# Kernel optimization log

Hardware: AMD Instinct MI355X
Metric: run time of the kernel (lower is better)

Reference implementation:

```python
import jax, jax.numpy as jnp
import numpy as np
import math

B, H, S, D = 2, 16, 2048, 72
D12 = D // 12  # freq dim per head per component
L_PREFIX, L_SEQ = 576, 512
THETA_T = 100.0


def _make_freqs():
    n = H * D12
    log_min, log_max = math.log(math.pi), math.log(10.0 * math.pi)
    f = jnp.exp(jnp.linspace(log_min, log_max, n + 1)[:-1])  # (H*D12,)
    freqs = jnp.stack([f, f]).reshape(2, D12, H)
    freqs = jnp.swapaxes(freqs, -1, -2)  # (2, H, D12)
    t = THETA_T ** (-jnp.arange(n, dtype=jnp.float32) / n)
    t_freqs = t.reshape(D12, H).T  # (H, D12)
    return freqs.astype(jnp.float32), t_freqs.astype(jnp.float32)


def setup_inputs() -> dict:
    key = jax.random.key(0)
    ks = jax.random.split(key, 8)
    freqs, t_freqs = _make_freqs()
    return {
        "q": jax.random.normal(ks[0], (B, H, S, D), dtype=jnp.float32),
        "k": jax.random.normal(ks[1], (B, H, S, D), dtype=jnp.float32),
        "v": jax.random.normal(ks[2], (B, H, S, D), dtype=jnp.float32),
        "pos": jax.random.uniform(ks[3], (B, S, 2), dtype=jnp.float32),
        "pos_orig": jax.random.uniform(ks[4], (B, S, 2), dtype=jnp.float32),
        "time": jax.random.uniform(ks[5], (B, S), dtype=jnp.float32),
        "freqs": freqs,
        "t_freqs": t_freqs,
        "scale": jax.random.uniform(ks[6], (H, 1, 1), dtype=jnpp_f32()) if False else jax.random.uniform(ks[6], (H, 1, 1), dtype=jnp.float32) + 0.5,
        "l_prefix": L_PREFIX,
        "l_seq": L_SEQ,
    }


def jnp_f32():
    return jnp.float32


def _fp_rope_theta(pos, pos_orig, time, freqs, t_freqs):
    # FPRoPE.forward: theta per token, per head. (B,S,H,5*D12)
    p = jnp.stack([pos_orig, pos], axis=2) * 2.0 - 1.0  # (B,S,2,2)
    th_w = p[..., 0][:, :, :, None, None] * freqs[0]  # (B,S,2,H,D12)
    th_h = p[..., 1][:, :, :, None, None] * freqs[1]  # (B,S,2,H,D12)
    th_t = time[:, :, None, None, None] * t_freqs      # (B,S,1,H,D12)
    theta = jnp.concatenate([th_h, th_w, th_t], axis=2)  # (B,S,5,H,D12)
    theta = jnp.transpose(theta, (0, 3, 1, 2, 4)).reshape(B, H, S, 5 * D12)
    return theta


def _apply_rotary(x, theta):
    d = theta.shape[-1]
    x1, x2, x3 = x[..., :d], x[..., d:2 * d], x[..., 2 * d:]
    c, s = jnp.cos(theta), jnp.sin(theta)
    return jnp.concatenate([x1 * c - x2 * s, x2 * c + x1 * s, x3], axis=-1)


def _block_mask(l_prefix, l_seq):
    # inference_query_causal_mask_mod: prefix attends to nothing; pokes causal;
    # queries attend to prefix+pokes (and self via qn==kn).
    idx = jnp.arange(S)
    qn = (idx - l_prefix)[:, None]
    kn = (idx - l_prefix)[None, :]
    return (qn >= 0) & ((qn == kn) | ((qn >= kn) & (qn < l_seq)) | ((kn < l_seq) & (qn >= l_seq)))


def reference(q, k, v, pos, pos_orig, time, freqs, t_freqs, scale, l_prefix, l_seq):
    theta = _fp_rope_theta(pos, pos_orig, time, freqs, t_freqs)
    q = _apply_rotary(q, theta)
    k = _apply_rotary(k, theta)
    # cosine-similarity QK rescaling (scale_for_cosine_sim)
    eps = 1e-6
    ss = jnp.sqrt(scale)  # (H,1,1) broadcasts over (B,H,S,1)
    q = q * (ss * jax.lax.rsqrt(jnp.sum(q * q, axis=-1, keepdims=True) + eps))
    k = k * (ss * jax.lax.rsqrt(jnp.sum(k * k, axis=-1, keepdims=True) + eps))
    mask = _block_mask(l_prefix, l_seq)  # (S,S)
    scores = jnp.einsum('bhqd,bhkd->bhqk', q, k)
    scores = jnp.where(mask, scores, jnp.float32(-1e30))
    probs = jax.nn.softmax(scores, axis=-1)
    # fully-masked rows (prefix queries) output zeros, matching flex_attention
    row_valid = jnp.any(mask, axis=-1)  # (S,)
    probs = jnp.where(row_valid[None, None, :, None], probs, 0.0)
    return jnp.einsum('bhqk,bhkd->bhqd', probs, v)
```

## Files before the change

kernel.cpp:

```cpp
#include <hip/hip_runtime.h>
#include <math.h>

#define B_ 2
#define H_ 16
#define S_ 2048
#define D_ 72
#define LP 576
#define WEND 1088
#define DP 96
#define DV 80
#define NQ (S_ - LP)

#define CBW 2688
#define LDSW (CBW + 128 + 32)

#define NPREP2 (B_ * H_ * S_ / 8)
#define NVT    (32 * B_ * H_)

typedef __bf16 bf16x8 __attribute__((ext_vector_type(8)));
typedef float f32x4 __attribute__((ext_vector_type(4)));

static __device__ __forceinline__ unsigned pack2bf(float a, float b) {
    __bf16 x = (__bf16)a, y = (__bf16)b;
    unsigned short ux = __builtin_bit_cast(unsigned short, x);
    unsigned short uy = __builtin_bit_cast(unsigned short, y);
    return (unsigned)ux | ((unsigned)uy << 16);
}

static __device__ __forceinline__ f32x4 mfma16(bf16x8 a, bf16x8 b, f32x4 c) {
    return __builtin_amdgcn_mfma_f32_16x16x32_bf16(a, b, c, 0, 0, 0);
}

__global__ __launch_bounds__(256) void pre_kernel(
    const float* __restrict__ q, const float* __restrict__ k,
    const float* __restrict__ v,
    const float* __restrict__ pos, const float* __restrict__ pos_orig,
    const float* __restrict__ time_, const float* __restrict__ freqs,
    const float* __restrict__ t_freqs, const float* __restrict__ scale,
    unsigned* __restrict__ qn, unsigned* __restrict__ kn,
    unsigned short* __restrict__ vt, float* __restrict__ out)
{
    __shared__ __align__(16) float tile[64 * 77];
    if (blockIdx.x < NPREP2) {
        unsigned short* shp = (unsigned short*)tile;
        const int wave = threadIdx.x >> 6;
        const int lane = threadIdx.x & 63;
        const int j = lane & 31;
        const int rw = wave * 2 + (lane >> 5);
        const int row = blockIdx.x * 8 + rw;
        const int s = row & (S_ - 1);
        const int h = (row >> 11) & (H_ - 1);
        const int b = row >> 15;
        const long base = (long)row * D_;
        const int p2 = (b * S_ + s) * 2;

        float oq1 = 0.f, oq2 = 0.f, ok1 = 0.f, ok2 = 0.f;
        float pq[6], pk[6];
        float ssq = 0.f, ssk = 0.f;
        if (j < 30) {
            const float x1q = q[base + j], x2q = q[base + j + 30];
            const float x1k = k[base + j], x2k = k[base + j + 30];
            const int g = j / 6, i = j - 6 * g;
            const float fh = freqs[96 + h * 6 + i];
            const float fw = freqs[h * 6 + i];
            const float ft = t_freqs[h * 6 + i];
            const float f  = (g < 2) ? fh : ((g < 4) ? fw : ft);
            const float by_o = pos_orig[p2 + 1] * 2.f - 1.f;
            const float by_p = pos[p2 + 1]      * 2.f - 1.f;
            const float bx_o = pos_orig[p2 + 0] * 2.f - 1.f;
            const float bx_p = pos[p2 + 0]      * 2.f - 1.f;
            const float bt   = time_[b * S_ + s];
            const float bv = (g == 0) ? by_o : (g == 1) ? by_p :
                             (g == 2) ? bx_o : (g == 3) ? bx_p : bt;
            float sn, cs;
            __sincosf(bv * f, &sn, &cs);
            oq1 = x1q * cs - x2q * sn;  oq2 = x2q * cs + x1q * sn;
            ok1 = x1k * cs - x2k * sn;  ok2 = x2k * cs + x1k * sn;
            ssq = oq1 * oq1 + oq2 * oq2;
            ssk = ok1 * ok1 + ok2 * ok2;
        } else {
            const int e0 = 60 + 6 * (j - 30);
            #pragma unroll
            for (int m = 0; m < 3; ++m) {
                const float2 a = *(const float2*)(q + base + e0 + 2 * m);
                const float2 c = *(const float2*)(k + base + e0 + 2 * m);
                pq[2 * m] = a.x; pq[2 * m + 1] = a.y;
                pk[2 * m] = c.x; pk[2 * m + 1] = c.y;
                ssq += a.x * a.x + a.y * a.y;
                ssk += c.x * c.x + c.y * c.y;
            }
        }
        #pragma unroll
        for (int m = 1; m < 32; m <<= 1) { ssq += __shfl_xor(ssq, m); ssk += __shfl_xor(ssk, m); }
        const float ss = sqrtf(scale[h]);
        const float fq = ss * rsqrtf(ssq + 1e-6f);
        const float fk = ss * rsqrtf(ssk + 1e-6f);

        unsigned short* sq_ = shp + rw * 96;
        unsigned short* sk_ = shp + 768 + rw * 96;
        if (j < 30) {
            sq_[j]      = __builtin_bit_cast(unsigned short, (__bf16)(oq1 * fq));
            sq_[j + 30] = __builtin_bit_cast(unsigned short, (__bf16)(oq2 * fq));
            sk_[j]      = __builtin_bit_cast(unsigned short, (__bf16)(ok1 * fk));
            sk_[j + 30] = __builtin_bit_cast(unsigned short, (__bf16)(ok2 * fk));
        } else {
            const int e0 = 60 + 6 * (j - 30);
            #pragma unroll
            for (int m = 0; m < 6; ++m) {
                sq_[e0 + m] = __builtin_bit_cast(unsigned short, (__bf16)(pq[m] * fq));
                sk_[e0 + m] = __builtin_bit_cast(unsigned short, (__bf16)(pk[m] * fk));
            }
        }
        __syncthreads();
        const int t = threadIdx.x;
        if (t < 192) {
            const int arr = t / 96, rem = t - arr * 96;
            const int rr = rem / 12, seg = rem - rr * 12;
            uint4 val = make_uint4(0u, 0u, 0u, 0u);
            if (seg < 9) val = ((const uint4*)(shp + arr * 768 + rr * 96))[seg];
            unsigned* dst = (arr ? kn : qn) + ((long)(blockIdx.x * 8 + rr)) * 48;
            ((uint4*)dst)[seg] = val;
        }
    } else {
        const int bx2 = blockIdx.x - NPREP2;
        const int st = bx2 & 31, bh = bx2 >> 5;
        const int s0 = st * 64;
        const int t = threadIdx.x;
        if (st < 9) {
            float4* o4 = (float4*)(out + (long)(bh * S_ + s0) * D_);
            for (int i = t; i < 1152; i += 256) o4[i] = make_float4(0.f, 0.f, 0.f, 0.f);
        }
        for (int i = t; i < 1152; i += 256) {
            const int r = i / 18, c = i - r * 18;
            const float4 g = ((const float4*)v)[((long)(bh * S_ + s0 + r) * 18) + c];
            float* d = &tile[r * 77 + c * 4];
            d[0] = g.x; d[1] = g.y; d[2] = g.z; d[3] = g.w;
        }
        __syncthreads();
        for (int i = t; i < 1280; i += 256) {
            const int dd = i >> 4, s4 = i & 15;
            float f0 = 0.f, f1 = 0.f, f2 = 0.f, f3 = 0.f;
            if (dd < D_) {
                f0 = tile[(s4 * 4 + 0) * 77 + dd];
                f1 = tile[(s4 * 4 + 1) * 77 + dd];
                f2 = tile[(s4 * 4 + 2) * 77 + dd];
                f3 = tile[(s4 * 4 + 3) * 77 + dd];
            }
            uint2 o; o.x = pack2bf(f0, f1); o.y = pack2bf(f2, f3);
            ((uint2*)vt)[((((long)bh * DV + dd) << 11) + s0 + s4 * 4) >> 2] = o;
        }
    }
}

__global__ __launch_bounds__(256) void attn_kernel(
    const unsigned short* __restrict__ qn, const unsigned short* __restrict__ kn,
    const unsigned short* __restrict__ vt, float* __restrict__ out)
{
    __shared__ __align__(16) unsigned lds[LDSW];
    const int bh = blockIdx.y;
    const int q0 = LP + blockIdx.x * 32;
    const int tid = threadIdx.x;
    const int w = tid >> 6, lane = tid & 63;
    const int quad = lane >> 4, l16 = lane & 15;
    const bool causal = (q0 < WEND);
    const int ntiles = causal ? ((q0 + 159) >> 7) : 9;

    const unsigned short* qn_b = qn + (((long)bh) << 11) * DP;
    const unsigned short* kn_b = kn + (((long)bh) << 11) * DP;
    const unsigned short* vt_b = vt + (long)bh * DV * S_;

    bf16x8 qf[2][3];
    #pragma unroll
    for (int m = 0; m < 2; ++m)
        #pragma unroll
        for (int c = 0; c < 3; ++c)
            qf[m][c] = *(const bf16x8*)(qn_b + (long)(q0 + 16 * m + l16) * DP + c * 32 + quad * 8);

    f32x4 o[2][5];
    float den[2][4];
    #pragma unroll
    for (int m = 0; m < 2; ++m) {
        #pragma unroll
        for (int dt = 0; dt < 5; ++dt) { o[m][dt][0]=0.f; o[m][dt][1]=0.f; o[m][dt][2]=0.f; o[m][dt][3]=0.f; }
        #pragma unroll
        for (int r = 0; r < 4; ++r) den[m][r] = 0.f;
    }

    unsigned short* Pw = (unsigned short*)lds + w * 640;

    for (int kt = 0; kt < ntiles; ++kt) {
        const int kb = kt * 128 + 32 * w;
        const bool masked = (kt == ntiles - 1);
        bf16x8 kf[2][3], vf[5];
        #pragma unroll
        for (int g = 0; g < 2; ++g)
            #pragma unroll
            for (int c = 0; c < 3; ++c)
                kf[g][c] = *(const bf16x8*)(kn_b + (long)(kb + 16 * g + l16) * DP + c * 32 + quad * 8);
        #pragma unroll
        for (int dt = 0; dt < 5; ++dt)
            vf[dt] = *(const bf16x8*)(vt_b + (((long)(dt * 16 + l16)) << 11) + kb + quad * 8);

        #pragma unroll
        for (int m = 0; m < 2; ++m) {
            f32x4 acc0, acc1;
            acc0[0]=0.f; acc0[1]=0.f; acc0[2]=0.f; acc0[3]=0.f;
            acc1[0]=0.f; acc1[1]=0.f; acc1[2]=0.f; acc1[3]=0.f;
            __builtin_amdgcn_s_setprio(1);
            #pragma unroll
            for (int c = 0; c < 3; ++c) {
                acc0 = mfma16(qf[m][c], kf[0][c], acc0);
                acc1 = mfma16(qf[m][c], kf[1][c], acc1);
            }
            __builtin_amdgcn_s_setprio(0);
            #pragma unroll
            for (int g = 0; g < 2; ++g) {
                const int ka = kb + 16 * g + l16;
                #pragma unroll
                for (int r = 0; r < 4; ++r) {
                    const int qa = q0 + 16 * m + quad * 4 + r;
                    float p = g ? acc1[r] : acc0[r];
                    float e = __expf(p);
                    if (masked) {
                        const bool valid = causal ? (ka <= qa) : (ka < WEND);
                        if (!valid) e = 0.f;
                    }
                    const __bf16 pb = (__bf16)e;
                    den[m][r] += (float)pb;
                    Pw[(quad * 4 + r) * 40 + 16 * g + l16] = __builtin_bit_cast(unsigned short, pb);
                }
            }
            const bf16x8 pa = *(const bf16x8*)(Pw + l16 * 40 + quad * 8);
            __builtin_amdgcn_s_setprio(1);
            #pragma unroll
            for (int dt = 0; dt < 5; ++dt)
                o[m][dt] = mfma16(pa, vf[dt], o[m][dt]);
            __builtin_amdgcn_s_setprio(0);
        }
    }

    #pragma unroll
    for (int m = 0; m < 2; ++m)
        #pragma unroll
        for (int r = 0; r < 4; ++r)
            #pragma unroll
            for (int x = 1; x < 16; x <<= 1) den[m][r] += __shfl_xor(den[m][r], x);

    __syncthreads();
    float* cb  = (float*)lds;
    float* db  = (float*)lds + CBW;
    float* PsD = (float*)lds + CBW + 128;
    if (l16 == 0)
        #pragma unroll
        for (int m = 0; m < 2; ++m)
            #pragma unroll
            for (int r = 0; r < 4; ++r)
                db[w * 32 + 16 * m + quad * 4 + r] = den[m][r];

    float ofin[5][2];
    #pragma unroll
    for (int dt = 0; dt < 5; ++dt) {
        __syncthreads();
        #pragma unroll
        for (int m = 0; m < 2; ++m)
            #pragma unroll
            for (int r = 0; r < 4; ++r)
                cb[w * 672 + (16 * m + quad * 4 + r) * 21 + l16] = o[m][dt][r];
        __syncthreads();
        #pragma unroll
        for (int r = 0; r < 2; ++r) {
            const int row = 8 * w + quad * 2 + r;
            ofin[dt][r] = cb[row * 21 + l16] + cb[672 + row * 21 + l16]
                        + cb[1344 + row * 21 + l16] + cb[2016 + row * 21 + l16];
        }
    }
    float dfin[2];
    #pragma unroll
    for (int r = 0; r < 2; ++r) {
        const int row = 8 * w + quad * 2 + r;
        dfin[r] = db[row] + db[32 + row] + db[64 + row] + db[96 + row];
    }

    if (!causal) {
        const int gq = w >> 1;
        bf16x8 qw[3];
        if (gq == 0) { qw[0] = qf[0][0]; qw[1] = qf[0][1]; qw[2] = qf[0][2]; }
        else         { qw[0] = qf[1][0]; qw[1] = qf[1][1]; qw[2] = qf[1][2]; }
        float sp = 0.f;
        #pragma unroll
        for (int c = 0; c < 3; ++c) {
            const bf16x8 kd = *(const bf16x8*)(kn_b + (long)(q0 + 16 * gq + l16) * DP + c * 32 + quad * 8);
            #pragma unroll
            for (int j = 0; j < 8; ++j) sp += (float)qw[c][j] * (float)kd[j];
        }
        sp += __shfl_xor(sp, 16);
        sp += __shfl_xor(sp, 32);
        if (quad == 0 && (w & 1) == 0) PsD[16 * gq + l16] = __expf(sp);
        __syncthreads();
        #pragma unroll
        for (int r = 0; r < 2; ++r) {
            const int row = 8 * w + quad * 2 + r;
            const float pd = PsD[row];
            dfin[r] += pd;
            const int qa = q0 + row;
            #pragma unroll
            for (int dt = 0; dt < 5; ++dt) {
                const unsigned short uv = vt_b[(((long)(dt * 16 + l16)) << 11) + qa];
                ofin[dt][r] += pd * (float)__builtin_bit_cast(__bf16, uv);
            }
        }
    }

    #pragma unroll
    for (int r = 0; r < 2; ++r) {
        const float inv = 1.f / dfin[r];
        const int qa = q0 + 8 * w + quad * 2 + r;
        float* orow = out + ((long)(bh * S_ + qa)) * D_;
        #pragma unroll
        for (int dt = 0; dt < 5; ++dt) {
            const int dim = dt * 16 + l16;
            if (dim < D_) orow[dim] = ofin[dt][r] * inv;
        }
    }
}

extern "C" void kernel_launch(void* const* d_in, const int* in_sizes, int n_in,
                              void* d_out, int out_size, void* d_ws, size_t ws_size,
                              hipStream_t stream) {
    const float* q        = (const float*)d_in[0];
    const float* k        = (const float*)d_in[1];
    const float* v        = (const float*)d_in[2];
    const float* pos      = (const float*)d_in[3];
    const float* pos_orig = (const float*)d_in[4];
    const float* time_    = (const float*)d_in[5];
    const float* freqs    = (const float*)d_in[6];
    const float* t_freqs  = (const float*)d_in[7];
    const float* scale    = (const float*)d_in[8];
    float* out = (float*)d_out;

    unsigned* qn = (unsigned*)d_ws;
    unsigned* kn = qn + (size_t)B_ * H_ * S_ * 48;
    unsigned short* vt = (unsigned short*)(kn + (size_t)B_ * H_ * S_ * 48);

    pre_kernel<<<dim3(NPREP2 + NVT), dim3(256), 0, stream>>>(
        q, k, v, pos, pos_orig, time_, freqs, t_freqs, scale, qn, kn, vt, out);
    attn_kernel<<<dim3(NQ / 32, B_ * H_), dim3(256), 0, stream>>>(
        (const unsigned short*)qn, (const unsigned short*)kn, vt, out);
}
```

Measured before the change: 188.1 us.

## Restructure attention as single-wave blocks with double-buffered async LDS staging

```diff
diff --git a/kernel.cpp b/kernel.cpp
--- a/kernel.cpp
+++ b/kernel.cpp
@@ -11,14 +11,12 @@
 #define DV 80
 #define NQ (S_ - LP)
 
-#define CBW 2688
-#define LDSW (CBW + 128 + 32)
-
 #define NPREP2 (B_ * H_ * S_ / 8)
 #define NVT    (32 * B_ * H_)
 
 typedef __bf16 bf16x8 __attribute__((ext_vector_type(8)));
 typedef float f32x4 __attribute__((ext_vector_type(4)));
+typedef short sh4   __attribute__((ext_vector_type(4)));
 
 static __device__ __forceinline__ unsigned pack2bf(float a, float b) {
     __bf16 x = (__bf16)a, y = (__bf16)b;
@@ -27,8 +25,15 @@
     return (unsigned)ux | ((unsigned)uy << 16);
 }
 
-static __device__ __forceinline__ f32x4 mfma16(bf16x8 a, bf16x8 b, f32x4 c) {
+static __device__ __forceinline__ f32x4 mfma32(bf16x8 a, bf16x8 b, f32x4 c) {
     return __builtin_amdgcn_mfma_f32_16x16x32_bf16(a, b, c, 0, 0, 0);
+}
+static __device__ __forceinline__ f32x4 mfma16k(sh4 a, sh4 b, f32x4 c) {
+    return __builtin_amdgcn_mfma_f32_16x16x16bf16_1k(a, b, c, 0, 0, 0);
+}
+static __device__ __forceinline__ void gll16(const void* g, void* l) {
+    __builtin_amdgcn_global_load_lds((const __attribute__((address_space(1))) unsigned*)g,
+                                     (__attribute__((address_space(3))) unsigned*)l, 16, 0, 0);
 }
 
 __global__ __launch_bounds__(256) void pre_kernel(
@@ -152,18 +157,18 @@
     }
 }
 
-__global__ __launch_bounds__(256) void attn_kernel(
+__global__ __launch_bounds__(64) void attn_kernel(
     const unsigned short* __restrict__ qn, const unsigned short* __restrict__ kn,
     const unsigned short* __restrict__ vt, float* __restrict__ out)
 {
-    __shared__ __align__(16) unsigned lds[LDSW];
+    __shared__ __align__(16) unsigned stage[2][2816];
+
     const int bh = blockIdx.y;
-    const int q0 = LP + blockIdx.x * 32;
-    const int tid = threadIdx.x;
-    const int w = tid >> 6, lane = tid & 63;
+    const int qw0 = LP + blockIdx.x * 32;
+    const int lane = threadIdx.x & 63;
     const int quad = lane >> 4, l16 = lane & 15;
-    const bool causal = (q0 < WEND);
-    const int ntiles = causal ? ((q0 + 159) >> 7) : 9;
+    const bool causal = (qw0 < WEND);
+    const int nt = causal ? (qw0 / 32 + 1) : (WEND / 32);
 
     const unsigned short* qn_b = qn + (((long)bh) << 11) * DP;
     const unsigned short* kn_b = kn + (((long)bh) << 11) * DP;
@@ -174,152 +179,155 @@
     for (int m = 0; m < 2; ++m)
         #pragma unroll
         for (int c = 0; c < 3; ++c)
-            qf[m][c] = *(const bf16x8*)(qn_b + (long)(q0 + 16 * m + l16) * DP + c * 32 + quad * 8);
+            qf[m][c] = *(const bf16x8*)(qn_b + (long)(qw0 + 16 * m + l16) * DP + c * 32 + quad * 8);
 
     f32x4 o[2][5];
-    float den[2][4];
-    #pragma unroll
-    for (int m = 0; m < 2; ++m) {
+    float den[2] = {0.f, 0.f};
+    #pragma unroll
+    for (int m = 0; m < 2; ++m)
         #pragma unroll
         for (int dt = 0; dt < 5; ++dt) { o[m][dt][0]=0.f; o[m][dt][1]=0.f; o[m][dt][2]=0.f; o[m][dt][3]=0.f; }
-        #pragma unroll
-        for (int r = 0; r < 4; ++r) den[m][r] = 0.f;
-    }
-
-    unsigned short* Pw = (unsigned short*)lds + w * 640;
-
-    for (int kt = 0; kt < ntiles; ++kt) {
-        const int kb = kt * 128 + 32 * w;
-        const bool masked = (kt == ntiles - 1);
-        bf16x8 kf[2][3], vf[5];
+
+    const unsigned short* pk[6];
+    const unsigned short* pv[5];
+    #pragma unroll
+    for (int g = 0; g < 2; ++g)
+        #pragma unroll
+        for (int c = 0; c < 3; ++c)
+            pk[g * 3 + c] = kn_b + (long)(16 * g + l16) * DP + c * 32 + quad * 8;
+    #pragma unroll
+    for (int dt = 0; dt < 5; ++dt)
+        pv[dt] = vt_b + (((long)(dt * 16 + l16)) << 11) + quad * 8;
+
+#define STAGE(BUF) do {                                                     \
+    _Pragma("unroll")                                                       \
+    for (int i_ = 0; i_ < 6; ++i_) {                                        \
+        gll16(pk[i_], (void*)&(BUF)[i_ * 256]);                             \
+        pk[i_] += 32 * DP;                                                  \
+    }                                                                       \
+    _Pragma("unroll")                                                       \
+    for (int i_ = 0; i_ < 5; ++i_) {                                        \
+        gll16(pv[i_], (void*)&(BUF)[(6 + i_) * 256]);                       \
+        pv[i_] += 32;                                                       \
+    }                                                                       \
+} while (0)
+
+    const int voffV = ((quad >> 1) * 16 + l16) * 8 + (quad & 1) * 4;
+    const int qa0 = qw0 + l16;
+
+    STAGE(stage[0]);
+
+    for (int t = 0; t < nt; ++t) {
+        const unsigned short* sb = (const unsigned short*)stage[t & 1];
+        asm volatile("s_waitcnt lgkmcnt(0)" ::: "memory");
+        if (t + 1 < nt) {
+            STAGE(stage[(t + 1) & 1]);
+            asm volatile("s_waitcnt vmcnt(11)" ::: "memory");
+        } else {
+            asm volatile("s_waitcnt vmcnt(0)" ::: "memory");
+        }
+
+        bf16x8 kf[2][3];
         #pragma unroll
         for (int g = 0; g < 2; ++g)
             #pragma unroll
             for (int c = 0; c < 3; ++c)
-                kf[g][c] = *(const bf16x8*)(kn_b + (long)(kb + 16 * g + l16) * DP + c * 32 + quad * 8);
-        #pragma unroll
-        for (int dt = 0; dt < 5; ++dt)
-            vf[dt] = *(const bf16x8*)(vt_b + (((long)(dt * 16 + l16)) << 11) + kb + quad * 8);
+                kf[g][c] = *(const bf16x8*)(sb + (g * 3 + c) * 512 + lane * 8);
+        sh4 vf[2][5];
+        #pragma unroll
+        for (int g = 0; g < 2; ++g)
+            #pragma unroll
+            for (int dt = 0; dt < 5; ++dt)
+                vf[g][dt] = *(const sh4*)(sb + 3072 + dt * 512 + g * 256 + voffV);
+
+        const bool maskedLast = causal && (t == nt - 1);
+        const int kb = t * 32;
 
         #pragma unroll
         for (int m = 0; m < 2; ++m) {
-            f32x4 acc0, acc1;
-            acc0[0]=0.f; acc0[1]=0.f; acc0[2]=0.f; acc0[3]=0.f;
-            acc1[0]=0.f; acc1[1]=0.f; acc1[2]=0.f; acc1[3]=0.f;
+            f32x4 s0, s1;
+            s0[0]=0.f; s0[1]=0.f; s0[2]=0.f; s0[3]=0.f;
+            s1[0]=0.f; s1[1]=0.f; s1[2]=0.f; s1[3]=0.f;
             __builtin_amdgcn_s_setprio(1);
             #pragma unroll
             for (int c = 0; c < 3; ++c) {
-                acc0 = mfma16(qf[m][c], kf[0][c], acc0);
-                acc1 = mfma16(qf[m][c], kf[1][c], acc1);
+                s0 = mfma32(kf[0][c], qf[m][c], s0);
+                s1 = mfma32(kf[1][c], qf[m][c], s1);
             }
             __builtin_amdgcn_s_setprio(0);
+            const int qa = qa0 + 16 * m;
             #pragma unroll
             for (int g = 0; g < 2; ++g) {
-                const int ka = kb + 16 * g + l16;
+                const f32x4 sg = g ? s1 : s0;
+                sh4 pa;
                 #pragma unroll
                 for (int r = 0; r < 4; ++r) {
-                    const int qa = q0 + 16 * m + quad * 4 + r;
-                    float p = g ? acc1[r] : acc0[r];
-                    float e = __expf(p);
-                    if (masked) {
-                        const bool valid = causal ? (ka <= qa) : (ka < WEND);
-                        if (!valid) e = 0.f;
+                    float e = __expf(sg[r]);
+                    if (maskedLast) {
+                        const int ka = kb + 16 * g + quad * 4 + r;
+                        if (ka > qa) e = 0.f;
                     }
                     const __bf16 pb = (__bf16)e;
-                    den[m][r] += (float)pb;
-                    Pw[(quad * 4 + r) * 40 + 16 * g + l16] = __builtin_bit_cast(unsigned short, pb);
+                    den[m] += (float)pb;
+                    pa[r] = __builtin_bit_cast(short, pb);
                 }
-            }
-            const bf16x8 pa = *(const bf16x8*)(Pw + l16 * 40 + quad * 8);
-            __builtin_amdgcn_s_setprio(1);
-            #pragma unroll
-            for (int dt = 0; dt < 5; ++dt)
-                o[m][dt] = mfma16(pa, vf[dt], o[m][dt]);
-            __builtin_amdgcn_s_setprio(0);
-        }
-    }
-
-    #pragma unroll
-    for (int m = 0; m < 2; ++m)
-        #pragma unroll
-        for (int r = 0; r < 4; ++r)
-            #pragma unroll
-            for (int x = 1; x < 16; x <<= 1) den[m][r] += __shfl_xor(den[m][r], x);
-
-    __syncthreads();
-    float* cb  = (float*)lds;
-    float* db  = (float*)lds + CBW;
-    float* PsD = (float*)lds + CBW + 128;
-    if (l16 == 0)
-        #pragma unroll
-        for (int m = 0; m < 2; ++m)
-            #pragma unroll
-            for (int r = 0; r < 4; ++r)
-                db[w * 32 + 16 * m + quad * 4 + r] = den[m][r];
-
-    float ofin[5][2];
-    #pragma unroll
-    for (int dt = 0; dt < 5; ++dt) {
-        __syncthreads();
-        #pragma unroll
-        for (int m = 0; m < 2; ++m)
-            #pragma unroll
-            for (int r = 0; r < 4; ++r)
-                cb[w * 672 + (16 * m + quad * 4 + r) * 21 + l16] = o[m][dt][r];
-        __syncthreads();
-        #pragma unroll
-        for (int r = 0; r < 2; ++r) {
-            const int row = 8 * w + quad * 2 + r;
-            ofin[dt][r] = cb[row * 21 + l16] + cb[672 + row * 21 + l16]
-                        + cb[1344 + row * 21 + l16] + cb[2016 + row * 21 + l16];
-        }
-    }
-    float dfin[2];
-    #pragma unroll
-    for (int r = 0; r < 2; ++r) {
-        const int row = 8 * w + quad * 2 + r;
-        dfin[r] = db[row] + db[32 + row] + db[64 + row] + db[96 + row];
-    }
-
+                __builtin_amdgcn_s_setprio(1);
+                #pragma unroll
+                for (int dt = 0; dt < 5; ++dt)
+                    o[m][dt] = mfma16k(pa, vf[g][dt], o[m][dt]);
+                __builtin_amdgcn_s_setprio(0);
+            }
+        }
+    }
+#undef STAGE
+
+    float pd[2] = {0.f, 0.f};
     if (!causal) {
-        const int gq = w >> 1;
-        bf16x8 qw[3];
-        if (gq == 0) { qw[0] = qf[0][0]; qw[1] = qf[0][1]; qw[2] = qf[0][2]; }
-        else         { qw[0] = qf[1][0]; qw[1] = qf[1][1]; qw[2] = qf[1][2]; }
-        float sp = 0.f;
-        #pragma unroll
-        for (int c = 0; c < 3; ++c) {
-            const bf16x8 kd = *(const bf16x8*)(kn_b + (long)(q0 + 16 * gq + l16) * DP + c * 32 + quad * 8);
-            #pragma unroll
-            for (int j = 0; j < 8; ++j) sp += (float)qw[c][j] * (float)kd[j];
-        }
-        sp += __shfl_xor(sp, 16);
-        sp += __shfl_xor(sp, 32);
-        if (quad == 0 && (w & 1) == 0) PsD[16 * gq + l16] = __expf(sp);
-        __syncthreads();
-        #pragma unroll
-        for (int r = 0; r < 2; ++r) {
-            const int row = 8 * w + quad * 2 + r;
-            const float pd = PsD[row];
-            dfin[r] += pd;
-            const int qa = q0 + row;
+        #pragma unroll
+        for (int m = 0; m < 2; ++m) {
+            float sp = 0.f;
+            #pragma unroll
+            for (int c = 0; c < 3; ++c) {
+                const bf16x8 kd = *(const bf16x8*)(kn_b + (long)(qw0 + 16 * m + l16) * DP + c * 32 + quad * 8);
+                #pragma unroll
+                for (int j = 0; j < 8; ++j) sp += (float)qf[m][c][j] * (float)kd[j];
+            }
+            sp += __shfl_xor(sp, 16);
+            sp += __shfl_xor(sp, 32);
+            pd[m] = __expf(sp);
+        }
+    }
+
+    float denf[2];
+    #pragma unroll
+    for (int m = 0; m < 2; ++m) {
+        float d = den[m];
+        d += __shfl_xor(d, 16);
+        d += __shfl_xor(d, 32);
+        denf[m] = causal ? d : (d + pd[m]);
+    }
+
+    #pragma unroll
+    for (int m = 0; m < 2; ++m) {
+        #pragma unroll
+        for (int r = 0; r < 4; ++r) {
+            const int row = 16 * m + quad * 4 + r;
+            const float df = __shfl(denf[m], quad * 4 + r);
+            const float inv = 1.f / df;
+            const int qa = qw0 + row;
+            float* orow = out + ((long)(bh * S_ + qa)) * D_;
+            float pdr = 0.f;
+            if (!causal) pdr = __shfl(pd[m], quad * 4 + r);
             #pragma unroll
             for (int dt = 0; dt < 5; ++dt) {
-                const unsigned short uv = vt_b[(((long)(dt * 16 + l16)) << 11) + qa];
-                ofin[dt][r] += pd * (float)__builtin_bit_cast(__bf16, uv);
-            }
-        }
-    }
-
-    #pragma unroll
-    for (int r = 0; r < 2; ++r) {
-        const float inv = 1.f / dfin[r];
-        const int qa = q0 + 8 * w + quad * 2 + r;
-        float* orow = out + ((long)(bh * S_ + qa)) * D_;
-        #pragma unroll
-        for (int dt = 0; dt < 5; ++dt) {
-            const int dim = dt * 16 + l16;
-            if (dim < D_) orow[dim] = ofin[dt][r] * inv;
+                float val = o[m][dt][r];
+                if (!causal) {
+                    const unsigned short uv = vt_b[(((long)(dt * 16 + l16)) << 11) + qa];
+                    val += pdr * (float)__builtin_bit_cast(__bf16, uv);
+                }
+                const int dim = dt * 16 + l16;
+                if (dim < D_) orow[dim] = val * inv;
+            }
         }
     }
 }
@@ -344,6 +352,6 @@
 
     pre_kernel<<<dim3(NPREP2 + NVT), dim3(256), 0, stream>>>(
         q, k, v, pos, pos_orig, time_, freqs, t_freqs, scale, qn, kn, vt, out);
-    attn_kernel<<<dim3(NQ / 32, B_ * H_), dim3(256), 0, stream>>>(
+    attn_kernel<<<dim3(NQ / 32, B_ * H_), dim3(64), 0, stream>>>(
         (const unsigned short*)qn, (const unsigned short*)kn, vt, out);
 }
```

Result: no change. 187.9 us (-0.1%).
